# Optimization experiments

Hardware: AMD Instinct MI355X
Metric: run time of the kernel (lower is better)

The kernel has to match this reference:

```python
import jax, jax.numpy as jnp
import numpy as np

IN_DIM = 128
OUT_DIM = 128
HEADS = 4
HEAD_DIM = OUT_DIM // HEADS
N_NODES = 50000
N_EDGES = 800000
NEG_SLOPE = 0.2
LN_EPS = 1e-5


def setup_inputs() -> dict:
    key = jax.random.key(0)
    ks = jax.random.split(key, 10)
    x = jax.random.normal(ks[0], (N_NODES, IN_DIM), dtype=jnp.float32)
    edge_index = jax.random.randint(ks[1], (2, N_EDGES), 0, N_NODES, dtype=jnp.int64)
    s = 1.0 / np.sqrt(IN_DIM)
    W_l = jax.random.normal(ks[2], (IN_DIM, HEADS * HEAD_DIM), dtype=jnp.float32) * s
    b_l = jnp.zeros((HEADS * HEAD_DIM,), dtype=jnp.float32)
    W_r = jax.random.normal(ks[3], (IN_DIM, HEADS * HEAD_DIM), dtype=jnp.float32) * s
    b_r = jnp.zeros((HEADS * HEAD_DIM,), dtype=jnp.float32)
    att = jax.random.normal(ks[4], (HEADS, HEAD_DIM), dtype=jnp.float32) * (1.0 / np.sqrt(HEAD_DIM))
    bias = jnp.zeros((HEADS * HEAD_DIM,), dtype=jnp.float32)
    gamma = jnp.ones((OUT_DIM,), dtype=jnp.float32)
    beta = jnp.zeros((OUT_DIM,), dtype=jnp.float32)
    return {"x": x, "edge_index": edge_index, "W_l": W_l, "b_l": b_l,
            "W_r": W_r, "b_r": b_r, "att": att, "bias": bias,
            "gamma": gamma, "beta": beta}


def reference(x, edge_index, W_l, b_l, W_r, b_r, att, bias, gamma, beta):
    N = x.shape[0]
    src, dst = edge_index[0], edge_index[1]
    # GATv2: separate linear transforms for source and target nodes
    xl = (x @ W_l + b_l).reshape(N, HEADS, HEAD_DIM)  # source / message features
    xr = (x @ W_r + b_r).reshape(N, HEADS, HEAD_DIM)  # target features
    # per-edge attention logits: a^T . leaky_relu(xl[src] + xr[dst])  -> [E, H]
    h = jax.nn.leaky_relu(xl[src] + xr[dst], NEG_SLOPE)
    e = jnp.einsum('ehd,hd->eh', h, att)
    # segment softmax over edges grouped by destination node
    m = jax.ops.segment_max(e, dst, num_segments=N)
    m = jnp.where(jnp.isfinite(m), m, 0.0)  # guard empty segments
    ex = jnp.exp(e - m[dst])
    denom = jax.ops.segment_sum(ex, dst, num_segments=N)
    alpha = ex / (denom[dst] + 1e-16)  # [E, H]
    # scatter-add weighted source features (dropout omitted: eval mode)
    out = jax.ops.segment_sum(alpha[:, :, None] * xl[src], dst, num_segments=N)
    out = out.reshape(N, HEADS * HEAD_DIM) + bias
    # residual (in_dim == out_dim) + LayerNorm
    out = out + x
    mu = out.mean(axis=-1, keepdims=True)
    var = ((out - mu) ** 2).mean(axis=-1, keepdims=True)
    return (out - mu) * jax.lax.rsqrt(var + LN_EPS) * gamma + beta
```

## Files before the change

kernel.cpp:

```cpp
#include <hip/hip_runtime.h>
#include <math.h>

#define NEG_SLOPE 0.2f
#define LN_EPS 1e-5f
#define CAP 64
#define HB 4096
#define RUN 56
#define XSTR 136
#define SMEM_BYTES (64 * XSTR * 2)

typedef __attribute__((ext_vector_type(8))) short s8v;
typedef __attribute__((ext_vector_type(8))) unsigned short u8v;
typedef __attribute__((ext_vector_type(4))) float f4v;

__device__ inline unsigned short f2bf(float f) {
    unsigned u = __float_as_uint(f);
    return (unsigned short)((u + 0x7FFFu + ((u >> 16) & 1u)) >> 16);
}
__device__ inline float bf2f(unsigned short h) {
    return __uint_as_float((unsigned)h << 16);
}

__global__ __launch_bounds__(256) void pre_scat_kernel(
    const int* __restrict__ src, const int* __restrict__ dst,
    const float* __restrict__ Wl, const float* __restrict__ Wr,
    unsigned short* __restrict__ packL, unsigned short* __restrict__ packR,
    unsigned* __restrict__ part, int* __restrict__ cntmat,
    int E, int NBKT) {
    const int bid = blockIdx.x, tid = threadIdx.x;
    if (bid < 2) {
        const float* W = bid ? Wr : Wl;
        unsigned short* pk = bid ? packR : packL;
        for (int idx = tid; idx < 16384; idx += 256) {
            int j = idx & 7;
            int lane = (idx >> 3) & 63;
            int ntt = idx >> 9;
            int t = ntt & 3, nt = ntt >> 2;
            int k = t * 32 + (lane >> 4) * 8 + j;
            int n = nt * 16 + (lane & 15);
            pk[idx] = f2bf(W[k * 128 + n]);
        }
        return;
    }
    __shared__ int cnt[256];
    const int sb = bid - 2;
    const int e0 = sb * HB;
    cnt[tid] = 0;
    __syncthreads();
    int es[16], ed[16];
    #pragma unroll
    for (int it = 0; it < 16; ++it) {
        int e = e0 + tid + it * 256;
        int s = 0, d = -1;
        if (e < E) {
            s = src[e];
            d = dst[e];
            atomicAdd(&cnt[d >> 8], 1);
        }
        es[it] = s; ed[it] = d;
    }
    __syncthreads();
    if (tid < NBKT) {
        int c = cnt[tid]; if (c > RUN) c = RUN;
        cntmat[(size_t)sb * NBKT + tid] = c;
        cnt[tid] = 0;
    }
    __syncthreads();
    #pragma unroll
    for (int it = 0; it < 16; ++it) {
        int d = ed[it];
        if (d >= 0) {
            int b = d >> 8;
            int r = atomicAdd(&cnt[b], 1);
            if (r < RUN)
                part[((size_t)sb * NBKT + b) * RUN + r] =
                    ((unsigned)(d & 255) << 16) | (unsigned)es[it];
        }
    }
}

__global__ __launch_bounds__(256, 4) void fill_tf_kernel(
    const unsigned* __restrict__ part, const int* __restrict__ cntmat,
    unsigned short* __restrict__ csr, int* __restrict__ deg,
    const float* __restrict__ x,
    const unsigned short* __restrict__ packL, const unsigned short* __restrict__ packR,
    const float* __restrict__ bl, const float* __restrict__ br,
    unsigned short* __restrict__ xl, float* __restrict__ xr,
    int N, int NBKT, int NSC, int TBS) {
    const int bid = blockIdx.x, tid = threadIdx.x;
    __shared__ __align__(16) char smem[SMEM_BYTES];

    if (bid < NBKT) {
        int* cur = (int*)smem;
        cur[tid] = 0;
        __syncthreads();
        const int b = bid;
        if (tid < NSC) {
            int cnt = cntmat[(size_t)tid * NBKT + b];
            const unsigned* seg = part + ((size_t)tid * NBKT + b) * RUN;
            for (int i = 0; i < cnt; ++i) {
                unsigned rec = seg[i];
                int dl = rec >> 16;
                int pos = atomicAdd(&cur[dl], 1);
                if (pos < CAP)
                    csr[(size_t)(b * 256 + dl) * CAP + pos] = (unsigned short)(rec & 0xFFFFu);
            }
        }
        __syncthreads();
        int node = b * 256 + tid;
        if (node < N) deg[node] = cur[tid];
        return;
    }

    unsigned short* xs = (unsigned short*)smem;
    const int rb = bid - NBKT;
    const int side = (rb >= TBS);
    const int tb = side ? rb - TBS : rb;
    const int blk0 = tb * 64;
    const unsigned short* __restrict__ pk = side ? packR : packL;
    const float* __restrict__ bb = side ? br : bl;

    #pragma unroll
    for (int it = 0; it < 8; ++it) {
        int slot = tid + it * 256;
        int row = slot >> 5, c4 = slot & 31;
        int node = blk0 + row;
        float4 v = make_float4(0.f, 0.f, 0.f, 0.f);
        if (node < N) v = *(const float4*)&x[(size_t)node * 128 + 4 * c4];
        ushort4 o;
        o.x = f2bf(v.x); o.y = f2bf(v.y); o.z = f2bf(v.z); o.w = f2bf(v.w);
        *(ushort4*)&xs[row * XSTR + 4 * c4] = o;
    }
    __syncthreads();

    const int wv = tid >> 6, lane = tid & 63;
    const int row = lane & 15, q = lane >> 4;
    const int node0 = blk0 + wv * 16;

    s8v afrag[4];
    #pragma unroll
    for (int t = 0; t < 4; ++t)
        afrag[t] = *(const s8v*)&xs[(wv * 16 + row) * XSTR + t * 32 + q * 8];

    f4v acc[8];
    #pragma unroll
    for (int nt = 0; nt < 8; ++nt) acc[nt] = (f4v){0.f, 0.f, 0.f, 0.f};

    #pragma unroll
    for (int t = 0; t < 4; ++t) {
        #pragma unroll
        for (int np = 0; np < 2; ++np) {
            s8v bfr[4];
            #pragma unroll
            for (int u = 0; u < 4; ++u)
                bfr[u] = *(const s8v*)&pk[(((np * 4 + u) * 4 + t) * 64 + lane) * 8];
            #pragma unroll
            for (int u = 0; u < 4; ++u)
                acc[np * 4 + u] = __builtin_amdgcn_mfma_f32_16x16x32_bf16(
                    afrag[t], bfr[u], acc[np * 4 + u], 0, 0, 0);
        }
    }

    #pragma unroll
    for (int nt = 0; nt < 8; ++nt) {
        float bcol = bb[nt * 16 + row];
        #pragma unroll
        for (int r2 = 0; r2 < 4; ++r2) {
            int nd = node0 + q * 4 + r2;
            if (nd < N) {
                float val = acc[nt][r2] + bcol;
                if (side) xr[(size_t)nd * 128 + nt * 16 + row] = val;
                else      xl[(size_t)nd * 128 + nt * 16 + row] = f2bf(val);
            }
        }
    }
}

__global__ __launch_bounds__(256) void gat_kernel(
    const int* __restrict__ deg_arr, const unsigned short* __restrict__ csr,
    const unsigned short* __restrict__ xl, const float* __restrict__ xr,
    const float* __restrict__ att, const float* __restrict__ x,
    const float* __restrict__ bias, const float* __restrict__ gamma,
    const float* __restrict__ beta, float* __restrict__ out, int N) {
    const int node = blockIdx.x * 4 + (threadIdx.x >> 6);
    const int lane = threadIdx.x & 63;
    if (node >= N) return;
    const int sub = lane & 15;
    const int eg  = lane >> 4;
    const int f0  = sub * 8;

    float xrf[8], av[8];
    {
        float4 a0 = *(const float4*)&xr[(size_t)node * 128 + f0];
        float4 a1 = *(const float4*)&xr[(size_t)node * 128 + f0 + 4];
        xrf[0] = a0.x; xrf[1] = a0.y; xrf[2] = a0.z; xrf[3] = a0.w;
        xrf[4] = a1.x; xrf[5] = a1.y; xrf[6] = a1.z; xrf[7] = a1.w;
        float4 c0 = *(const float4*)&att[f0];
        float4 c1 = *(const float4*)&att[f0 + 4];
        av[0] = c0.x; av[1] = c0.y; av[2] = c0.z; av[3] = c0.w;
        av[4] = c1.x; av[5] = c1.y; av[6] = c1.z; av[7] = c1.w;
    }

    int dg = deg_arr[node]; if (dg > CAP) dg = CAP;
    const unsigned short* crow = csr + (size_t)node * CAP;

    float den = 0.f;
    float acc[8] = {0.f, 0.f, 0.f, 0.f, 0.f, 0.f, 0.f, 0.f};

    u8v buf0 = {0,0,0,0,0,0,0,0}, buf1 = {0,0,0,0,0,0,0,0}, buf2 = {0,0,0,0,0,0,0,0};
    if (eg < dg)      buf0 = *(const u8v*)&xl[(size_t)crow[eg] * 128 + f0];
    if (eg + 4 < dg)  buf1 = *(const u8v*)&xl[(size_t)crow[eg + 4] * 128 + f0];
    if (eg + 8 < dg)  buf2 = *(const u8v*)&xl[(size_t)crow[eg + 8] * 128 + f0];

    for (int i = eg; i < dg; i += 4) {
        u8v cur = buf0;
        buf0 = buf1;
        buf1 = buf2;
        if (i + 12 < dg) buf2 = *(const u8v*)&xl[(size_t)crow[i + 12] * 128 + f0];

        float xf[8];
        float p = 0.f;
        #pragma unroll
        for (int j = 0; j < 8; ++j) {
            xf[j] = bf2f(cur[j]);
            float t = xf[j] + xrf[j];
            float h = fmaxf(t, t * NEG_SLOPE);
            p = fmaf(h, av[j], p);
        }
        p += __shfl_xor(p, 1);
        p += __shfl_xor(p, 2);
        float w = __expf(p);
        den += w;
        #pragma unroll
        for (int j = 0; j < 8; ++j) acc[j] = fmaf(w, xf[j], acc[j]);
    }

    den += __shfl_xor(den, 16); den += __shfl_xor(den, 32);
    #pragma unroll
    for (int j = 0; j < 8; ++j) {
        acc[j] += __shfl_xor(acc[j], 16);
        acc[j] += __shfl_xor(acc[j], 32);
    }

    const float inv = 1.0f / (den + 1e-16f);
    float v[8];
    {
        float4 b0 = *(const float4*)&bias[f0];
        float4 b1 = *(const float4*)&bias[f0 + 4];
        float4 r0 = *(const float4*)&x[(size_t)node * 128 + f0];
        float4 r1 = *(const float4*)&x[(size_t)node * 128 + f0 + 4];
        const float bbf[8] = {b0.x, b0.y, b0.z, b0.w, b1.x, b1.y, b1.z, b1.w};
        const float rrf[8] = {r0.x, r0.y, r0.z, r0.w, r1.x, r1.y, r1.z, r1.w};
        #pragma unroll
        for (int j = 0; j < 8; ++j) v[j] = acc[j] * inv + bbf[j] + rrf[j];
    }

    float s = v[0] + v[1] + v[2] + v[3] + v[4] + v[5] + v[6] + v[7];
    s += __shfl_xor(s, 1); s += __shfl_xor(s, 2);
    s += __shfl_xor(s, 4); s += __shfl_xor(s, 8);
    const float mu = s * (1.0f / 128.0f);

    float d[8], vs = 0.f;
    #pragma unroll
    for (int j = 0; j < 8; ++j) { d[j] = v[j] - mu; vs = fmaf(d[j], d[j], vs); }
    vs += __shfl_xor(vs, 1); vs += __shfl_xor(vs, 2);
    vs += __shfl_xor(vs, 4); vs += __shfl_xor(vs, 8);
    const float rstd = rsqrtf(vs * (1.0f / 128.0f) + LN_EPS);

    if (eg == 0) {
        float4 g0 = *(const float4*)&gamma[f0];
        float4 g1 = *(const float4*)&gamma[f0 + 4];
        float4 e0 = *(const float4*)&beta[f0];
        float4 e1 = *(const float4*)&beta[f0 + 4];
        float4 o0, o1;
        o0.x = d[0] * rstd * g0.x + e0.x;  o0.y = d[1] * rstd * g0.y + e0.y;
        o0.z = d[2] * rstd * g0.z + e0.z;  o0.w = d[3] * rstd * g0.w + e0.w;
        o1.x = d[4] * rstd * g1.x + e1.x;  o1.y = d[5] * rstd * g1.y + e1.y;
        o1.z = d[6] * rstd * g1.z + e1.z;  o1.w = d[7] * rstd * g1.w + e1.w;
        *(float4*)&out[(size_t)node * 128 + f0]     = o0;
        *(float4*)&out[(size_t)node * 128 + f0 + 4] = o1;
    }
}

extern "C" void kernel_launch(void* const* d_in, const int* in_sizes, int n_in,
                              void* d_out, int out_size, void* d_ws, size_t ws_size,
                              hipStream_t stream) {
    const float* x     = (const float*)d_in[0];
    const int*   ei    = (const int*)d_in[1];
    const float* Wl    = (const float*)d_in[2];
    const float* bl    = (const float*)d_in[3];
    const float* Wr    = (const float*)d_in[4];
    const float* br    = (const float*)d_in[5];
    const float* att   = (const float*)d_in[6];
    const float* bias  = (const float*)d_in[7];
    const float* gamma = (const float*)d_in[8];
    const float* beta  = (const float*)d_in[9];

    const int N = in_sizes[0] / 128;
    const int E = in_sizes[1] / 2;
    const int* src = ei;
    const int* dst = ei + E;

    const int NBKT = (N + 255) >> 8;
    const int NSC  = (E + HB - 1) / HB;
    const int TBS  = (N + 63) / 64;

    char* w = (char*)d_ws;
    unsigned short* xl    = (unsigned short*)w;  w += (size_t)N * 128 * sizeof(unsigned short);
    float*          xr    = (float*)w;           w += (size_t)N * 128 * sizeof(float);
    unsigned short* packL = (unsigned short*)w;  w += 16384 * sizeof(unsigned short);
    unsigned short* packR = (unsigned short*)w;  w += 16384 * sizeof(unsigned short);
    unsigned*       part  = (unsigned*)w;        w += (size_t)NSC * NBKT * RUN * sizeof(unsigned);
    int*            cntmat= (int*)w;             w += (size_t)NSC * NBKT * sizeof(int);
    unsigned short* csr   = (unsigned short*)w;  w += (size_t)N * CAP * sizeof(unsigned short);
    int*            deg   = (int*)w;             w += (size_t)N * sizeof(int);

    pre_scat_kernel<<<2 + NSC, 256, 0, stream>>>(
        src, dst, Wl, Wr, packL, packR, part, cntmat, E, NBKT);
    fill_tf_kernel<<<NBKT + 2 * TBS, 256, 0, stream>>>(
        part, cntmat, csr, deg, x, packL, packR, bl, br, xl, xr, N, NBKT, NSC, TBS);
    gat_kernel<<<(N + 3) / 4, 256, 0, stream>>>(
        deg, csr, xl, xr, att, x, bias, gamma, beta, (float*)d_out, N);
}
```

Baseline: 178.0 us.

## Store xl/xr in fp16, use packed half math for edge logits, deepen gather prefetch

Projected source and target features are now stored as fp16 instead of bf16 and fp32, which halves the xr footprint. The per-edge leaky-relu and attention dot product run as packed half2 operations. The gather loop issues eight neighbor-row loads up front instead of keeping a rolling three-deep buffer, to expose more memory-level parallelism. The risks are lower precision in the logits, since the packed half accumulation may lose accuracy, and higher register pressure from the eight float4 buffers.

```diff
diff --git a/kernel.cpp b/kernel.cpp
--- a/kernel.cpp
+++ b/kernel.cpp
@@ -10,15 +10,12 @@
 #define SMEM_BYTES (64 * XSTR * 2)
 
 typedef __attribute__((ext_vector_type(8))) short s8v;
-typedef __attribute__((ext_vector_type(8))) unsigned short u8v;
 typedef __attribute__((ext_vector_type(4))) float f4v;
+typedef _Float16 h2 __attribute__((ext_vector_type(2)));
 
 __device__ inline unsigned short f2bf(float f) {
     unsigned u = __float_as_uint(f);
     return (unsigned short)((u + 0x7FFFu + ((u >> 16) & 1u)) >> 16);
-}
-__device__ inline float bf2f(unsigned short h) {
-    return __uint_as_float((unsigned)h << 16);
 }
 
 __global__ __launch_bounds__(256) void pre_scat_kernel(
@@ -85,7 +82,7 @@
     const float* __restrict__ x,
     const unsigned short* __restrict__ packL, const unsigned short* __restrict__ packR,
     const float* __restrict__ bl, const float* __restrict__ br,
-    unsigned short* __restrict__ xl, float* __restrict__ xr,
+    _Float16* __restrict__ xl, _Float16* __restrict__ xr,
     int N, int NBKT, int NSC, int TBS) {
     const int bid = blockIdx.x, tid = threadIdx.x;
     __shared__ __align__(16) char smem[SMEM_BYTES];
@@ -119,6 +116,7 @@
     const int blk0 = tb * 64;
     const unsigned short* __restrict__ pk = side ? packR : packL;
     const float* __restrict__ bb = side ? br : bl;
+    _Float16* __restrict__ dsth = side ? xr : xl;
 
     #pragma unroll
     for (int it = 0; it < 8; ++it) {
@@ -167,18 +165,39 @@
         #pragma unroll
         for (int r2 = 0; r2 < 4; ++r2) {
             int nd = node0 + q * 4 + r2;
-            if (nd < N) {
-                float val = acc[nt][r2] + bcol;
-                if (side) xr[(size_t)nd * 128 + nt * 16 + row] = val;
-                else      xl[(size_t)nd * 128 + nt * 16 + row] = f2bf(val);
-            }
-        }
-    }
+            if (nd < N)
+                dsth[(size_t)nd * 128 + nt * 16 + row] = (_Float16)(acc[nt][r2] + bcol);
+        }
+    }
+}
+
+__device__ inline void edge_body(float4 raw, const h2* xr2, const h2* av2,
+                                 h2 ns2, float& den, float* acc) {
+    float fr[4];
+    fr[0] = raw.x; fr[1] = raw.y; fr[2] = raw.z; fr[3] = raw.w;
+    h2 pacc = (h2){(_Float16)0.f, (_Float16)0.f};
+    float xf[8];
+    #pragma unroll
+    for (int j = 0; j < 4; ++j) {
+        h2 c = __builtin_bit_cast(h2, fr[j]);
+        h2 t = c + xr2[j];
+        h2 hh = __builtin_elementwise_max(t, t * ns2);
+        pacc = pacc + hh * av2[j];
+        xf[2 * j]     = (float)c.x;
+        xf[2 * j + 1] = (float)c.y;
+    }
+    float p = (float)pacc.x + (float)pacc.y;
+    p += __shfl_xor(p, 1);
+    p += __shfl_xor(p, 2);
+    float w = __expf(p);
+    den += w;
+    #pragma unroll
+    for (int j = 0; j < 8; ++j) acc[j] = fmaf(w, xf[j], acc[j]);
 }
 
 __global__ __launch_bounds__(256) void gat_kernel(
     const int* __restrict__ deg_arr, const unsigned short* __restrict__ csr,
-    const unsigned short* __restrict__ xl, const float* __restrict__ xr,
+    const _Float16* __restrict__ xl, const _Float16* __restrict__ xr,
     const float* __restrict__ att, const float* __restrict__ x,
     const float* __restrict__ bias, const float* __restrict__ gamma,
     const float* __restrict__ beta, float* __restrict__ out, int N) {
@@ -189,50 +208,42 @@
     const int eg  = lane >> 4;
     const int f0  = sub * 8;
 
-    float xrf[8], av[8];
+    h2 xr2[4], av2[4];
     {
-        float4 a0 = *(const float4*)&xr[(size_t)node * 128 + f0];
-        float4 a1 = *(const float4*)&xr[(size_t)node * 128 + f0 + 4];
-        xrf[0] = a0.x; xrf[1] = a0.y; xrf[2] = a0.z; xrf[3] = a0.w;
-        xrf[4] = a1.x; xrf[5] = a1.y; xrf[6] = a1.z; xrf[7] = a1.w;
+        float4 xrw = *(const float4*)&xr[(size_t)node * 128 + f0];
+        float fw[4]; fw[0] = xrw.x; fw[1] = xrw.y; fw[2] = xrw.z; fw[3] = xrw.w;
+        #pragma unroll
+        for (int j = 0; j < 4; ++j) xr2[j] = __builtin_bit_cast(h2, fw[j]);
         float4 c0 = *(const float4*)&att[f0];
         float4 c1 = *(const float4*)&att[f0 + 4];
-        av[0] = c0.x; av[1] = c0.y; av[2] = c0.z; av[3] = c0.w;
-        av[4] = c1.x; av[5] = c1.y; av[6] = c1.z; av[7] = c1.w;
-    }
+        av2[0] = (h2){(_Float16)c0.x, (_Float16)c0.y};
+        av2[1] = (h2){(_Float16)c0.z, (_Float16)c0.w};
+        av2[2] = (h2){(_Float16)c1.x, (_Float16)c1.y};
+        av2[3] = (h2){(_Float16)c1.z, (_Float16)c1.w};
+    }
+    const h2 ns2 = (h2){(_Float16)NEG_SLOPE, (_Float16)NEG_SLOPE};
 
     int dg = deg_arr[node]; if (dg > CAP) dg = CAP;
     const unsigned short* crow = csr + (size_t)node * CAP;
 
+    float4 bufv[8];
+    #pragma unroll
+    for (int k = 0; k < 8; ++k) {
+        bufv[k] = make_float4(0.f, 0.f, 0.f, 0.f);
+        int i = eg + 4 * k;
+        if (i < dg) bufv[k] = *(const float4*)&xl[(size_t)crow[i] * 128 + f0];
+    }
+
     float den = 0.f;
     float acc[8] = {0.f, 0.f, 0.f, 0.f, 0.f, 0.f, 0.f, 0.f};
 
-    u8v buf0 = {0,0,0,0,0,0,0,0}, buf1 = {0,0,0,0,0,0,0,0}, buf2 = {0,0,0,0,0,0,0,0};
-    if (eg < dg)      buf0 = *(const u8v*)&xl[(size_t)crow[eg] * 128 + f0];
-    if (eg + 4 < dg)  buf1 = *(const u8v*)&xl[(size_t)crow[eg + 4] * 128 + f0];
-    if (eg + 8 < dg)  buf2 = *(const u8v*)&xl[(size_t)crow[eg + 8] * 128 + f0];
-
-    for (int i = eg; i < dg; i += 4) {
-        u8v cur = buf0;
-        buf0 = buf1;
-        buf1 = buf2;
-        if (i + 12 < dg) buf2 = *(const u8v*)&xl[(size_t)crow[i + 12] * 128 + f0];
-
-        float xf[8];
-        float p = 0.f;
-        #pragma unroll
-        for (int j = 0; j < 8; ++j) {
-            xf[j] = bf2f(cur[j]);
-            float t = xf[j] + xrf[j];
-            float h = fmaxf(t, t * NEG_SLOPE);
-            p = fmaf(h, av[j], p);
-        }
-        p += __shfl_xor(p, 1);
-        p += __shfl_xor(p, 2);
-        float w = __expf(p);
-        den += w;
-        #pragma unroll
-        for (int j = 0; j < 8; ++j) acc[j] = fmaf(w, xf[j], acc[j]);
+    #pragma unroll
+    for (int k = 0; k < 8; ++k)
+        if (eg + 4 * k < dg) edge_body(bufv[k], xr2, av2, ns2, den, acc);
+
+    for (int i = eg + 32; i < dg; i += 4) {
+        float4 raw = *(const float4*)&xl[(size_t)crow[i] * 128 + f0];
+        edge_body(raw, xr2, av2, ns2, den, acc);
     }
 
     den += __shfl_xor(den, 16); den += __shfl_xor(den, 32);
@@ -306,8 +317,8 @@
     const int TBS  = (N + 63) / 64;
 
     char* w = (char*)d_ws;
-    unsigned short* xl    = (unsigned short*)w;  w += (size_t)N * 128 * sizeof(unsigned short);
-    float*          xr    = (float*)w;           w += (size_t)N * 128 * sizeof(float);
+    _Float16*       xl    = (_Float16*)w;        w += (size_t)N * 128 * sizeof(_Float16);
+    _Float16*       xr    = (_Float16*)w;        w += (size_t)N * 128 * sizeof(_Float16);
     unsigned short* packL = (unsigned short*)w;  w += 16384 * sizeof(unsigned short);
     unsigned short* packR = (unsigned short*)w;  w += 16384 * sizeof(unsigned short);
     unsigned*       part  = (unsigned*)w;        w += (size_t)NSC * NBKT * RUN * sizeof(unsigned);
```

Measured after the change: 173.6 us. -2.5%, faster.
